# Optimization experiments

Measured on AMD Instinct MI355X. Metric: run time of the kernel, lower is better.

The kernel has to match this reference:

```python
import jax, jax.numpy as jnp
import numpy as np

SAMPLE_RATE = 16000
FREQ_LOW = 200.0
FREQ_HIGH = 1200.0
# deterministic stand-in for random.uniform(freq_low, freq_high): midpoint
FREQUENCY = 0.5 * (FREQ_LOW + FREQ_HIGH)  # 700 Hz
CUTOFF = FREQUENCY / SAMPLE_RATE          # normalized cutoff, as in cutoff_frequency()
Q = 0.70710678  # standard Butterworth-like quality factor for biquad highpass


def _biquad_highpass_coeffs(cutoff, q):
    # standard audio-EQ-cookbook highpass biquad, cutoff normalized to sample rate
    w0 = 2.0 * np.pi * cutoff
    cw, sw = np.cos(w0), np.sin(w0)
    alpha = sw / (2.0 * q)
    b0 = (1.0 + cw) / 2.0
    b1 = -(1.0 + cw)
    b2 = (1.0 + cw) / 2.0
    a0 = 1.0 + alpha
    a1 = -2.0 * cw
    a2 = 1.0 - alpha
    return (np.float32(b0 / a0), np.float32(b1 / a0), np.float32(b2 / a0),
            np.float32(a1 / a0), np.float32(a2 / a0))


def setup_inputs() -> dict:
    key = jax.random.key(0)
    B, C, T = 128, 2, 65536
    audio = jax.random.normal(key, (B, C, T), dtype=jnp.float32)
    return {"audio": audio}


def reference(audio) -> jnp.ndarray:
    b0, b1, b2, a1, a2 = _biquad_highpass_coeffs(CUTOFF, Q)
    x_t = jnp.moveaxis(audio, -1, 0)  # [T, B, C] for scan over time
    zero = jnp.zeros(x_t.shape[1:], dtype=audio.dtype)

    def step(carry, x):
        x1, x2, y1, y2 = carry
        # IIR biquad difference equation
        y = b0 * x + b1 * x1 + b2 * x2 - a1 * y1 - a2 * y2
        return (x, x1, y, y1), y

    _, y_t = jax.lax.scan(step, (zero, zero, zero, zero), x_t)
    return jnp.moveaxis(y_t, 0, -1)  # [B, C, T]
```

## Files before the change

kernel.cpp:

```cpp
#include <hip/hip_runtime.h>
#include <math.h>


#define T_LEN   65536
#define L_CHUNK 64
#define W_WARM  64
#define TS      32
#define BLK     64
#define NT      ((W_WARM + L_CHUNK) / TS)
#define CHUNK_SHIFT 10
#define ROWS    64
#define WLDS    (ROWS * TS)

__device__ __forceinline__ void lds_fence() {
    asm volatile("s_waitcnt lgkmcnt(0)" ::: "memory");
}

__device__ __forceinline__ void load_tile(const float* __restrict__ x,
                                          int cg0, int cbase, int tile,
                                          float4* pf, int lane)
{
    #pragma unroll
    for (int p = 0; p < 8; ++p) {
        int q   = lane + (p << 6);
        int seg = q >> 3;
        int g   = q & 7;
        int pos = (cg0 + seg) * L_CHUNK - W_WARM + tile * TS + (g << 2);
        float4 v = make_float4(0.f, 0.f, 0.f, 0.f);
        if (pos >= cbase)
            v = *(const float4*)(x + pos);
        pf[p] = v;
    }
}

__global__ __launch_bounds__(BLK, 4)
void hp_biquad_kernel(const float* __restrict__ x, float* __restrict__ y,
                      float b0, float b1, float b2, float a1, float a2)
{
    __shared__ float wlds[WLDS];
    const int lane = threadIdx.x;
    const int cg0  = blockIdx.x * ROWS;
    const int cbase = (cg0 >> CHUNK_SHIFT) * T_LEN;

    float4 pf[2][8];
    load_tile(x, cg0, cbase, 0, pf[0], lane);
    load_tile(x, cg0, cbase, 1, pf[1], lane);

    float x1 = 0.f, x2 = 0.f, y1 = 0.f, y2 = 0.f;

    #pragma unroll
    for (int tile = 0; tile < NT; ++tile) {
        float4* cur = pf[tile & 1];

        #pragma unroll
        for (int p = 0; p < 8; ++p) {
            int q    = lane + (p << 6);
            int seg  = q >> 3;
            int g    = q & 7;
            int slot = ((g + seg) & 7) << 2;
            *(float4*)&wlds[seg * TS + slot] = cur[p];
        }
        lds_fence();

        if (tile + 2 < NT)
            load_tile(x, cg0, cbase, tile + 2, cur, lane);

        float4 r[8];
        #pragma unroll
        for (int g = 0; g < 8; ++g) {
            int slot = ((g + lane) & 7) << 2;
            r[g] = *(float4*)&wlds[lane * TS + slot];
        }

        #pragma unroll
        for (int g = 0; g < 8; ++g) {
            float4 v = r[g];
            float yv;
            yv = b0 * v.x + b1 * x1 + b2 * x2 - a1 * y1 - a2 * y2;
            x2 = x1; x1 = v.x; y2 = y1; y1 = yv; v.x = yv;
            yv = b0 * v.y + b1 * x1 + b2 * x2 - a1 * y1 - a2 * y2;
            x2 = x1; x1 = v.y; y2 = y1; y1 = yv; v.y = yv;
            yv = b0 * v.z + b1 * x1 + b2 * x2 - a1 * y1 - a2 * y2;
            x2 = x1; x1 = v.z; y2 = y1; y1 = yv; v.z = yv;
            yv = b0 * v.w + b1 * x1 + b2 * x2 - a1 * y1 - a2 * y2;
            x2 = x1; x1 = v.w; y2 = y1; y1 = yv; v.w = yv;
            r[g] = v;
        }

        if (tile >= W_WARM / TS) {
            #pragma unroll
            for (int g = 0; g < 8; ++g) {
                int slot = ((g + lane) & 7) << 2;
                *(float4*)&wlds[lane * TS + slot] = r[g];
            }
            lds_fence();
            #pragma unroll
            for (int p = 0; p < 8; ++p) {
                int q    = lane + (p << 6);
                int seg  = q >> 3;
                int g    = q & 7;
                int slot = ((g + seg) & 7) << 2;
                float4 v = *(float4*)&wlds[seg * TS + slot];
                int pos  = (cg0 + seg) * L_CHUNK - W_WARM + tile * TS + (g << 2);
                *(float4*)(y + pos) = v;
            }
        }
        lds_fence();
    }
}

extern "C" void kernel_launch(void* const* d_in, const int* in_sizes, int n_in,
                              void* d_out, int out_size, void* d_ws, size_t ws_size,
                              hipStream_t stream)
{
    const float* x = (const float*)d_in[0];
    float* y = (float*)d_out;

    const double SR = 16000.0, FLO = 200.0, FHI = 1200.0;
    const double freq   = 0.5 * (FLO + FHI);
    const double cutoff = freq / SR;
    const double q      = 0.70710678;
    const double w0 = 2.0 * M_PI * cutoff;
    const double cw = cos(w0), sw = sin(w0);
    const double alpha = sw / (2.0 * q);
    const double b0 = (1.0 + cw) / 2.0;
    const double b1 = -(1.0 + cw);
    const double b2 = (1.0 + cw) / 2.0;
    const double a0 = 1.0 + alpha;
    const double a1 = -2.0 * cw;
    const double a2 = 1.0 - alpha;
    const float fb0 = (float)(b0 / a0), fb1 = (float)(b1 / a0), fb2 = (float)(b2 / a0);
    const float fa1 = (float)(a1 / a0), fa2 = (float)(a2 / a0);

    const int total  = 128 * 2 * T_LEN;
    const int chunks = total / L_CHUNK;
    const int blocks = chunks / BLK;

    hp_biquad_kernel<<<blocks, BLK, 0, stream>>>(x, y, fb0, fb1, fb2, fa1, fa2);
    (void)in_sizes; (void)n_in; (void)out_size; (void)d_ws; (void)ws_size;
}
```

Baseline: 134.0 us.

## Load input tiles straight into LDS with global_load_lds and double buffer

Input tiles now go from global memory directly into two LDS buffers through global_load_lds. This replaces the register prefetch followed by an LDS store. Waits are driven by vmcnt counts so each tile's filtering overlaps the next tile's DMA. Output is staged in the two LDS buffers and written once with coalesced stores at the end, instead of a transpose after every tile. Zero-padding at channel starts is handled by clamping the address and zeroing the first lane's warm-up data. This depends on correct vmcnt accounting and the LDS swizzle layout matching the DMA lane mapping.

Measured after the change: 115.4 us. 1.16x faster.

```diff
diff --git a/kernel.cpp b/kernel.cpp
--- a/kernel.cpp
+++ b/kernel.cpp
@@ -2,110 +2,118 @@
 #include <math.h>
 
 
-#define T_LEN   65536
-#define L_CHUNK 64
-#define W_WARM  64
-#define TS      32
-#define BLK     64
-#define NT      ((W_WARM + L_CHUNK) / TS)
-#define CHUNK_SHIFT 10
-#define ROWS    64
-#define WLDS    (ROWS * TS)
+#define T_LEN    65536
+#define L_CHUNK  64
+#define W_WARM   64
+#define TS       32
+#define BLK      64
+#define ROWS     64
+#define BUF_F    (ROWS * TS)
+#define BLOCKS_PER_CH 16
+
+#define WAITVM(n) asm volatile("s_waitcnt vmcnt(" #n ")" ::: "memory")
 
 __device__ __forceinline__ void lds_fence() {
     asm volatile("s_waitcnt lgkmcnt(0)" ::: "memory");
 }
 
-__device__ __forceinline__ void load_tile(const float* __restrict__ x,
-                                          int cg0, int cbase, int tile,
-                                          float4* pf, int lane)
+__device__ __forceinline__ void dma_tile(const float* __restrict__ x,
+                                         int base_f, int tile, float* buf)
 {
     #pragma unroll
-    for (int p = 0; p < 8; ++p) {
-        int q   = lane + (p << 6);
-        int seg = q >> 3;
-        int g   = q & 7;
-        int pos = (cg0 + seg) * L_CHUNK - W_WARM + tile * TS + (g << 2);
-        float4 v = make_float4(0.f, 0.f, 0.f, 0.f);
-        if (pos >= cbase)
-            v = *(const float4*)(x + pos);
-        pf[p] = v;
+    for (int i = 0; i < 8; ++i) {
+        int pos = base_f + i * 512 + tile * TS;
+        pos = pos < 0 ? 0 : pos;
+        __builtin_amdgcn_global_load_lds(
+            (__attribute__((address_space(1))) void*)(void*)(x + pos),
+            (__attribute__((address_space(3))) void*)(buf + i * 256),
+            16, 0, 0);
+    }
+}
+
+template <bool WARM>
+__device__ __forceinline__ void tile_filter(float* buf, int lane, bool ch0,
+    float c_b0, float c_b1, float c_b2, float c_a1, float c_a2,
+    float& x1, float& x2, float& y1, float& y2)
+{
+    float4 r[8];
+    #pragma unroll
+    for (int g = 0; g < 8; ++g)
+        r[g] = *(float4*)&buf[(lane * 8 + ((g + lane) & 7)) * 4];
+
+    if (WARM && ch0) {
+        #pragma unroll
+        for (int g = 0; g < 8; ++g) r[g] = make_float4(0.f, 0.f, 0.f, 0.f);
+    }
+
+    #pragma unroll
+    for (int g = 0; g < 8; ++g) {
+        float4 v = r[g];
+        float yv;
+        yv = c_b0*v.x + c_b1*x1 + c_b2*x2 - c_a1*y1 - c_a2*y2;
+        x2 = x1; x1 = v.x; y2 = y1; y1 = yv; v.x = yv;
+        yv = c_b0*v.y + c_b1*x1 + c_b2*x2 - c_a1*y1 - c_a2*y2;
+        x2 = x1; x1 = v.y; y2 = y1; y1 = yv; v.y = yv;
+        yv = c_b0*v.z + c_b1*x1 + c_b2*x2 - c_a1*y1 - c_a2*y2;
+        x2 = x1; x1 = v.z; y2 = y1; y1 = yv; v.z = yv;
+        yv = c_b0*v.w + c_b1*x1 + c_b2*x2 - c_a1*y1 - c_a2*y2;
+        x2 = x1; x1 = v.w; y2 = y1; y1 = yv; v.w = yv;
+        if (!WARM) r[g] = v;
+    }
+
+    if (!WARM) {
+        #pragma unroll
+        for (int g = 0; g < 8; ++g)
+            *(float4*)&buf[(lane * 8 + ((g + lane) & 7)) * 4] = r[g];
     }
 }
 
 __global__ __launch_bounds__(BLK, 4)
 void hp_biquad_kernel(const float* __restrict__ x, float* __restrict__ y,
-                      float b0, float b1, float b2, float a1, float a2)
+                      float c_b0, float c_b1, float c_b2, float c_a1, float c_a2)
 {
-    __shared__ float wlds[WLDS];
+    __shared__ float bufA[BUF_F];
+    __shared__ float bufB[BUF_F];
     const int lane = threadIdx.x;
     const int cg0  = blockIdx.x * ROWS;
-    const int cbase = (cg0 >> CHUNK_SHIFT) * T_LEN;
+    const bool ch0 = ((blockIdx.x & (BLOCKS_PER_CH - 1)) == 0) && (lane == 0);
 
-    float4 pf[2][8];
-    load_tile(x, cg0, cbase, 0, pf[0], lane);
-    load_tile(x, cg0, cbase, 1, pf[1], lane);
+    const int l0  = lane >> 3;
+    const int j0  = ((lane & 7) - l0) & 7;
+    const int bsf = (cg0 + l0) * L_CHUNK - W_WARM + j0 * 4;
 
     float x1 = 0.f, x2 = 0.f, y1 = 0.f, y2 = 0.f;
 
+    dma_tile(x, bsf, 0, bufA);
+    dma_tile(x, bsf, 1, bufB);
+
+    WAITVM(8);
+    tile_filter<true>(bufA, lane, ch0, c_b0, c_b1, c_b2, c_a1, c_a2, x1, x2, y1, y2);
+    lds_fence();
+    dma_tile(x, bsf, 2, bufA);
+
+    WAITVM(8);
+    tile_filter<true>(bufB, lane, ch0, c_b0, c_b1, c_b2, c_a1, c_a2, x1, x2, y1, y2);
+    lds_fence();
+    dma_tile(x, bsf, 3, bufB);
+
+    WAITVM(8);
+    tile_filter<false>(bufA, lane, ch0, c_b0, c_b1, c_b2, c_a1, c_a2, x1, x2, y1, y2);
+
+    WAITVM(0);
+    tile_filter<false>(bufB, lane, ch0, c_b0, c_b1, c_b2, c_a1, c_a2, x1, x2, y1, y2);
+    lds_fence();
+
+    const int ybase = cg0 * L_CHUNK + lane * 4;
     #pragma unroll
-    for (int tile = 0; tile < NT; ++tile) {
-        float4* cur = pf[tile & 1];
-
-        #pragma unroll
-        for (int p = 0; p < 8; ++p) {
-            int q    = lane + (p << 6);
-            int seg  = q >> 3;
-            int g    = q & 7;
-            int slot = ((g + seg) & 7) << 2;
-            *(float4*)&wlds[seg * TS + slot] = cur[p];
-        }
-        lds_fence();
-
-        if (tile + 2 < NT)
-            load_tile(x, cg0, cbase, tile + 2, cur, lane);
-
-        float4 r[8];
-        #pragma unroll
-        for (int g = 0; g < 8; ++g) {
-            int slot = ((g + lane) & 7) << 2;
-            r[g] = *(float4*)&wlds[lane * TS + slot];
-        }
-
-        #pragma unroll
-        for (int g = 0; g < 8; ++g) {
-            float4 v = r[g];
-            float yv;
-            yv = b0 * v.x + b1 * x1 + b2 * x2 - a1 * y1 - a2 * y2;
-            x2 = x1; x1 = v.x; y2 = y1; y1 = yv; v.x = yv;
-            yv = b0 * v.y + b1 * x1 + b2 * x2 - a1 * y1 - a2 * y2;
-            x2 = x1; x1 = v.y; y2 = y1; y1 = yv; v.y = yv;
-            yv = b0 * v.z + b1 * x1 + b2 * x2 - a1 * y1 - a2 * y2;
-            x2 = x1; x1 = v.z; y2 = y1; y1 = yv; v.z = yv;
-            yv = b0 * v.w + b1 * x1 + b2 * x2 - a1 * y1 - a2 * y2;
-            x2 = x1; x1 = v.w; y2 = y1; y1 = yv; v.w = yv;
-            r[g] = v;
-        }
-
-        if (tile >= W_WARM / TS) {
-            #pragma unroll
-            for (int g = 0; g < 8; ++g) {
-                int slot = ((g + lane) & 7) << 2;
-                *(float4*)&wlds[lane * TS + slot] = r[g];
-            }
-            lds_fence();
-            #pragma unroll
-            for (int p = 0; p < 8; ++p) {
-                int q    = lane + (p << 6);
-                int seg  = q >> 3;
-                int g    = q & 7;
-                int slot = ((g + seg) & 7) << 2;
-                float4 v = *(float4*)&wlds[seg * TS + slot];
-                int pos  = (cg0 + seg) * L_CHUNK - W_WARM + tile * TS + (g << 2);
-                *(float4*)(y + pos) = v;
-            }
-        }
-        lds_fence();
+    for (int p = 0; p < 16; ++p) {
+        int q   = lane + p * 64;
+        int seg = q >> 4;
+        int jj  = q & 15;
+        float* b = (jj < 8) ? bufA : bufB;
+        int g   = jj & 7;
+        float4 v = *(float4*)&b[(seg * 8 + ((g + seg) & 7)) * 4];
+        *(float4*)(y + ybase + p * 256) = v;
     }
 }
 
@@ -134,7 +142,7 @@
 
     const int total  = 128 * 2 * T_LEN;
     const int chunks = total / L_CHUNK;
-    const int blocks = chunks / BLK;
+    const int blocks = chunks / ROWS;
 
     hp_biquad_kernel<<<blocks, BLK, 0, stream>>>(x, y, fb0, fb1, fb2, fa1, fa2);
     (void)in_sizes; (void)n_in; (void)out_size; (void)d_ws; (void)ws_size;
```
